# Kernel optimization log

Hardware: AMD Instinct MI355X
Metric: run time of the kernel (lower is better)

Reference implementation:

```python
import jax, jax.numpy as jnp
import numpy as np

N, DIN, DOUT = 8192, 4096, 4096

def setup_inputs() -> dict:
    key = jax.random.key(0)
    k1, k2 = jax.random.split(key)
    x = jax.random.normal(k1, (N, DIN), dtype=jnp.float32)
    # ternary-ish weights; forward applies sign() via STE anyway
    weight = jax.random.normal(k2, (DOUT, DIN), dtype=jnp.float32)
    bias = jnp.zeros((DOUT,), dtype=jnp.float32)
    scale = jnp.ones((1,), dtype=jnp.float32)  # scale_init = 1.0
    return {"x": x, "weight": weight, "bias": bias, "scale": scale}


def reference(x, weight, bias, scale):
    # STE sign-quantization: value is sign(weight) in {-1,0,1},
    # gradient flows to weight as identity.
    w = weight - jax.lax.stop_gradient(weight - jnp.sign(weight))
    # fused ternary matmul + scale + bias: out = scale * (x @ w.T + bias)
    # (backward in the torch code scales grad for x, w, AND bias, implying
    #  bias sits inside the scale multiplier)
    return scale[0] * (jnp.matmul(x, w.T) + bias)
```

## Files before the change

### kernel.cpp

```cpp
#include <hip/hip_runtime.h>
#include <hip/hip_bf16.h>
#include <stdint.h>

#define M_DIM 8192
#define K_DIM 4096
#define N_DIM 4096

typedef int intx4  __attribute__((ext_vector_type(4)));
typedef int intx16 __attribute__((ext_vector_type(16)));

__global__ void cvt_fused_i8_kernel(const float* __restrict__ x,
                                    const float* __restrict__ w,
                                    signed char* __restrict__ xb,
                                    signed char* __restrict__ wb,
                                    float* __restrict__ row_scale) {
    const int b   = blockIdx.x;
    const int tid = threadIdx.x;
    if (b < M_DIM) {
        __shared__ float wmax[4];
        const float* xr = x + (size_t)b * K_DIM;
        float4 v[4];
#pragma unroll
        for (int i = 0; i < 4; ++i)
            v[i] = *(const float4*)(xr + tid * 4 + i * 1024);

        float am = 0.f;
#pragma unroll
        for (int i = 0; i < 4; ++i) {
            am = fmaxf(am, fabsf(v[i].x)); am = fmaxf(am, fabsf(v[i].y));
            am = fmaxf(am, fabsf(v[i].z)); am = fmaxf(am, fabsf(v[i].w));
        }
#pragma unroll
        for (int off = 32; off > 0; off >>= 1)
            am = fmaxf(am, __shfl_xor(am, off));
        if ((tid & 63) == 0) wmax[tid >> 6] = am;
        __syncthreads();
        am = fmaxf(fmaxf(wmax[0], wmax[1]), fmaxf(wmax[2], wmax[3]));
        am = fmaxf(am, 1e-30f);

        const float inv = 127.f / am;
#pragma unroll
        for (int i = 0; i < 4; ++i) {
            union { signed char c[4]; uint32_t u; } r;
            const float* vf = (const float*)&v[i];
#pragma unroll
            for (int k = 0; k < 4; ++k) {
                int q = (int)rintf(vf[k] * inv);
                q = q > 127 ? 127 : (q < -127 ? -127 : q);
                r.c[k] = (signed char)q;
            }
            *(uint32_t*)(xb + (size_t)b * K_DIM + tid * 4 + i * 1024) = r.u;
        }
        if (tid == 0) row_scale[b] = am * (1.f / 127.f);
    } else {
        size_t t = ((size_t)(b - M_DIM) * blockDim.x + tid) * 8;
        float4 a = *(const float4*)(w + t);
        float4 c = *(const float4*)(w + t + 4);
        union { signed char s[8]; uint2 u; } r;
        r.s[0] = (a.x > 0.f) - (a.x < 0.f); r.s[1] = (a.y > 0.f) - (a.y < 0.f);
        r.s[2] = (a.z > 0.f) - (a.z < 0.f); r.s[3] = (a.w > 0.f) - (a.w < 0.f);
        r.s[4] = (c.x > 0.f) - (c.x < 0.f); r.s[5] = (c.y > 0.f) - (c.y < 0.f);
        r.s[6] = (c.z > 0.f) - (c.z < 0.f); r.s[7] = (c.w > 0.f) - (c.w < 0.f);
        *(uint2*)(wb + t) = r.u;
    }
}

__device__ __forceinline__ void gld_lds16(const void* g, void* l) {
    __builtin_amdgcn_global_load_lds(
        (const __attribute__((address_space(1))) void*)g,
        (__attribute__((address_space(3))) void*)l,
        16, 0, 0);
}

__global__ void __launch_bounds__(512, 2)
gemm_i8_kernel(const signed char* __restrict__ A,
               const signed char* __restrict__ B,
               const float* __restrict__ bias,
               const float* __restrict__ scale,
               const float* __restrict__ row_scale,
               float* __restrict__ out) {
    __shared__ __attribute__((aligned(16))) signed char sA[3][256 * 64];
    __shared__ __attribute__((aligned(16))) signed char sB[3][256 * 64];

    const int tid  = threadIdx.x;
    const int lane = tid & 63;
    const int wave = tid >> 6;
    const int wm = wave >> 2;
    const int wn = wave & 3;
    const int r5 = lane & 31;
    const int hi = lane >> 5;

    const int bid = blockIdx.x;
    const int swz = (bid & 7) * 64 + (bid >> 3);
    const int rowBase = (swz >> 4) * 256;
    const int colBase = (swz & 15) * 256;

    const int sc   = (lane & 3) ^ ((lane >> 3) & 3) ^ ((wave & 1) << 1);
    const int srow = wave * 16 + (lane >> 2);
    const signed char* gA0 = A + (size_t)(rowBase + srow) * K_DIM + sc * 16;
    const signed char* gA1 = gA0 + (size_t)128 * K_DIM;
    const signed char* gB0 = B + (size_t)(colBase + srow) * K_DIM + sc * 16;
    const signed char* gB1 = gB0 + (size_t)128 * K_DIM;
    const int ldsR0 = wave * 1024;
    const int ldsR1 = 8192 + wave * 1024;

    const int fsw = ((r5 >> 1) & 3) ^ (((r5 >> 4) & 1) << 1);
    const int ckE = ((hi + 0) ^ fsw) * 16;
    const int ckO = ((hi + 2) ^ fsw) * 16;
    const int aOff = (wm * 128 + r5) * 64;
    const int bOff = (wn * 64 + r5) * 64;

    intx16 acc[4][2] = {};

#pragma unroll
    for (int s = 0; s < 2; ++s) {
        const size_t kg = (size_t)s * 64;
        gld_lds16(gA0 + kg, &sA[s][ldsR0]);
        gld_lds16(gA1 + kg, &sA[s][ldsR1]);
        gld_lds16(gB0 + kg, &sB[s][ldsR0]);
        gld_lds16(gB1 + kg, &sB[s][ldsR1]);
    }
    asm volatile("s_waitcnt vmcnt(4)" ::: "memory");
    __builtin_amdgcn_s_barrier();

    int sr = 0;
    int sw = 2;
    for (int t = 0; t < 64; ++t) {
        const signed char* sAb = sA[sr];
        const signed char* sBb = sB[sr];

        intx4 fa[4], fb[2];
#pragma unroll
        for (int mt = 0; mt < 4; ++mt)
            fa[mt] = *(const intx4*)(sAb + aOff + mt * 2048 + ckE);
#pragma unroll
        for (int nt = 0; nt < 2; ++nt)
            fb[nt] = *(const intx4*)(sBb + bOff + nt * 2048 + ckE);
        __builtin_amdgcn_sched_barrier(0);

        intx4 oa[4], ob[2];
#pragma unroll
        for (int mt = 0; mt < 4; ++mt)
            oa[mt] = *(const intx4*)(sAb + aOff + mt * 2048 + ckO);
#pragma unroll
        for (int nt = 0; nt < 2; ++nt)
            ob[nt] = *(const intx4*)(sBb + bOff + nt * 2048 + ckO);
        if (t <= 61) {
            const size_t kg = (size_t)(t + 2) * 64;
            gld_lds16(gA0 + kg, &sA[sw][ldsR0]);
            gld_lds16(gA1 + kg, &sA[sw][ldsR1]);
            gld_lds16(gB0 + kg, &sB[sw][ldsR0]);
            gld_lds16(gB1 + kg, &sB[sw][ldsR1]);
        }
        __builtin_amdgcn_sched_barrier(0);

        __builtin_amdgcn_s_setprio(1);
#pragma unroll
        for (int mt = 0; mt < 4; ++mt)
#pragma unroll
            for (int nt = 0; nt < 2; ++nt)
                acc[mt][nt] = __builtin_amdgcn_mfma_i32_32x32x32_i8(
                    fa[mt], fb[nt], acc[mt][nt], 0, 0, 0);
        __builtin_amdgcn_s_setprio(0);
        __builtin_amdgcn_sched_barrier(0);

        __builtin_amdgcn_s_setprio(1);
#pragma unroll
        for (int mt = 0; mt < 4; ++mt)
#pragma unroll
            for (int nt = 0; nt < 2; ++nt)
                acc[mt][nt] = __builtin_amdgcn_mfma_i32_32x32x32_i8(
                    oa[mt], ob[nt], acc[mt][nt], 0, 0, 0);
        __builtin_amdgcn_s_setprio(0);
        __builtin_amdgcn_sched_barrier(0);

        if (t <= 61)      asm volatile("s_waitcnt vmcnt(4)" ::: "memory");
        else if (t == 62) asm volatile("s_waitcnt vmcnt(0)" ::: "memory");
        __builtin_amdgcn_s_barrier();

        sr = (sr == 2) ? 0 : sr + 1;
        sw = (sw == 2) ? 0 : sw + 1;
    }

    const float s = scale[0];
#pragma unroll
    for (int nt = 0; nt < 2; ++nt) {
        const int gcol = colBase + wn * 64 + nt * 32 + r5;
        const float bv = bias[gcol];
#pragma unroll
        for (int mt = 0; mt < 4; ++mt) {
#pragma unroll
            for (int q = 0; q < 4; ++q) {
                const int row0 = rowBase + wm * 128 + mt * 32 + q * 8 + hi * 4;
                const float4 rs4 = *(const float4*)(row_scale + row0);
                const float rs[4] = {rs4.x, rs4.y, rs4.z, rs4.w};
#pragma unroll
                for (int r = 0; r < 4; ++r)
                    __builtin_nontemporal_store(
                        s * ((float)acc[mt][nt][q * 4 + r] * rs[r] + bv),
                        out + (size_t)(row0 + r) * N_DIM + gcol);
            }
        }
    }
}

__global__ void fallback_kernel(const float* __restrict__ x,
                                const float* __restrict__ w,
                                const float* __restrict__ bias,
                                const float* __restrict__ scale,
                                float* __restrict__ out) {
    int col = blockIdx.x * 64 + (threadIdx.x & 63);
    int row = blockIdx.y * 4 + (threadIdx.x >> 6);
    const float* xr = x + (size_t)row * K_DIM;
    const float* wr = w + (size_t)col * K_DIM;
    float acc = 0.f;
    for (int k = 0; k < K_DIM; k += 4) {
        float4 a = *(const float4*)(xr + k);
        float4 b = *(const float4*)(wr + k);
        acc += a.x * (b.x > 0.f ? 1.f : (b.x < 0.f ? -1.f : 0.f));
        acc += a.y * (b.y > 0.f ? 1.f : (b.y < 0.f ? -1.f : 0.f));
        acc += a.z * (b.z > 0.f ? 1.f : (b.z < 0.f ? -1.f : 0.f));
        acc += a.w * (b.w > 0.f ? 1.f : (b.w < 0.f ? -1.f : 0.f));
    }
    out[(size_t)row * N_DIM + col] = scale[0] * (acc + bias[col]);
}

extern "C" void kernel_launch(void* const* d_in, const int* in_sizes, int n_in,
                              void* d_out, int out_size, void* d_ws, size_t ws_size,
                              hipStream_t stream) {
    const float* x     = (const float*)d_in[0];
    const float* w     = (const float*)d_in[1];
    const float* bias  = (const float*)d_in[2];
    const float* scale = (const float*)d_in[3];
    float* out = (float*)d_out;

    const size_t xb_bytes = (size_t)M_DIM * K_DIM;
    const size_t wb_bytes = (size_t)N_DIM * K_DIM;
    const size_t need = xb_bytes + wb_bytes + M_DIM * sizeof(float);

    if (ws_size >= need) {
        signed char* xb = (signed char*)d_ws;
        signed char* wb = xb + xb_bytes;
        float* row_scale = (float*)(wb + wb_bytes);
        const unsigned w_blocks = (unsigned)((size_t)N_DIM * K_DIM / 8 / 256);
        cvt_fused_i8_kernel<<<dim3(M_DIM + w_blocks), 256, 0, stream>>>(
            x, w, xb, wb, row_scale);
        gemm_i8_kernel<<<dim3((M_DIM / 256) * (N_DIM / 256)), 512, 0, stream>>>(
            xb, wb, bias, scale, row_scale, out);
    } else {
        dim3 grid(N_DIM / 64, M_DIM / 4);
        fallback_kernel<<<grid, 256, 0, stream>>>(x, w, bias, scale, out);
    }
}
```

Measured before the change: 395.9 us.

## Use 4 waves per block with 128x128 per-wave tiles in int8 GEMM

The block drops from 8 waves to 4, and each wave now computes a 128x128 output sub-tile (4x4 MFMA tiles) instead of 128x64. This raises register-level reuse of the A and B fragments read from LDS and halves the LDS fragment reads per MFMA. Each thread issues twice as many global-to-LDS loads, with the swizzled loading adjusted to match. It doubles the accumulator registers and lowers occupancy to one block per CU, which may hurt latency hiding.

```diff
diff --git a/kernel.cpp b/kernel.cpp
--- a/kernel.cpp
+++ b/kernel.cpp
@@ -72,7 +72,7 @@
         16, 0, 0);
 }
 
-__global__ void __launch_bounds__(512, 2)
+__global__ void __launch_bounds__(256, 1)
 gemm_i8_kernel(const signed char* __restrict__ A,
                const signed char* __restrict__ B,
                const float* __restrict__ bias,
@@ -85,8 +85,8 @@
     const int tid  = threadIdx.x;
     const int lane = tid & 63;
     const int wave = tid >> 6;
-    const int wm = wave >> 2;
-    const int wn = wave & 3;
+    const int wm = wave >> 1;
+    const int wn = wave & 1;
     const int r5 = lane & 31;
     const int hi = lane >> 5;
 
@@ -95,32 +95,39 @@
     const int rowBase = (swz >> 4) * 256;
     const int colBase = (swz & 15) * 256;
 
-    const int sc   = (lane & 3) ^ ((lane >> 3) & 3) ^ ((wave & 1) << 1);
-    const int srow = wave * 16 + (lane >> 2);
-    const signed char* gA0 = A + (size_t)(rowBase + srow) * K_DIM + sc * 16;
-    const signed char* gA1 = gA0 + (size_t)128 * K_DIM;
-    const signed char* gB0 = B + (size_t)(colBase + srow) * K_DIM + sc * 16;
-    const signed char* gB1 = gB0 + (size_t)128 * K_DIM;
-    const int ldsR0 = wave * 1024;
-    const int ldsR1 = 8192 + wave * 1024;
+    const int scE = (lane & 3) ^ ((lane >> 3) & 3);
+    const int scO = scE ^ 2;
+    const int srow = wave * 64 + (lane >> 2);
+    const signed char* gAe = A + (size_t)(rowBase + srow) * K_DIM + scE * 16;
+    const signed char* gAo = A + (size_t)(rowBase + srow) * K_DIM + scO * 16;
+    const signed char* gBe = B + (size_t)(colBase + srow) * K_DIM + scE * 16;
+    const signed char* gBo = B + (size_t)(colBase + srow) * K_DIM + scO * 16;
+    const int ldsW = (wave * 64) * 64;
+
+#define STAGE(slot, kt)                                                        \
+    do {                                                                       \
+        const size_t kg_ = (size_t)(kt) * 64;                                  \
+        gld_lds16(gAe + kg_,                  &sA[slot][ldsW]);                \
+        gld_lds16(gAo + kg_ + 16 * K_DIM,     &sA[slot][ldsW + 1024]);         \
+        gld_lds16(gAe + kg_ + 32 * K_DIM,     &sA[slot][ldsW + 2048]);         \
+        gld_lds16(gAo + kg_ + 48 * K_DIM,     &sA[slot][ldsW + 3072]);         \
+        gld_lds16(gBe + kg_,                  &sB[slot][ldsW]);                \
+        gld_lds16(gBo + kg_ + 16 * K_DIM,     &sB[slot][ldsW + 1024]);         \
+        gld_lds16(gBe + kg_ + 32 * K_DIM,     &sB[slot][ldsW + 2048]);         \
+        gld_lds16(gBo + kg_ + 48 * K_DIM,     &sB[slot][ldsW + 3072]);         \
+    } while (0)
 
     const int fsw = ((r5 >> 1) & 3) ^ (((r5 >> 4) & 1) << 1);
     const int ckE = ((hi + 0) ^ fsw) * 16;
     const int ckO = ((hi + 2) ^ fsw) * 16;
     const int aOff = (wm * 128 + r5) * 64;
-    const int bOff = (wn * 64 + r5) * 64;
-
-    intx16 acc[4][2] = {};
-
-#pragma unroll
-    for (int s = 0; s < 2; ++s) {
-        const size_t kg = (size_t)s * 64;
-        gld_lds16(gA0 + kg, &sA[s][ldsR0]);
-        gld_lds16(gA1 + kg, &sA[s][ldsR1]);
-        gld_lds16(gB0 + kg, &sB[s][ldsR0]);
-        gld_lds16(gB1 + kg, &sB[s][ldsR1]);
-    }
-    asm volatile("s_waitcnt vmcnt(4)" ::: "memory");
+    const int bOff = (wn * 128 + r5) * 64;
+
+    intx16 acc[4][4] = {};
+
+    STAGE(0, 0);
+    STAGE(1, 1);
+    asm volatile("s_waitcnt vmcnt(8)" ::: "memory");
     __builtin_amdgcn_s_barrier();
 
     int sr = 0;
@@ -129,36 +136,30 @@
         const signed char* sAb = sA[sr];
         const signed char* sBb = sB[sr];
 
-        intx4 fa[4], fb[2];
+        intx4 fa[4], fb[4];
 #pragma unroll
         for (int mt = 0; mt < 4; ++mt)
             fa[mt] = *(const intx4*)(sAb + aOff + mt * 2048 + ckE);
 #pragma unroll
-        for (int nt = 0; nt < 2; ++nt)
+        for (int nt = 0; nt < 4; ++nt)
             fb[nt] = *(const intx4*)(sBb + bOff + nt * 2048 + ckE);
         __builtin_amdgcn_sched_barrier(0);
 
-        intx4 oa[4], ob[2];
+        intx4 oa[4], ob[4];
 #pragma unroll
         for (int mt = 0; mt < 4; ++mt)
             oa[mt] = *(const intx4*)(sAb + aOff + mt * 2048 + ckO);
 #pragma unroll
-        for (int nt = 0; nt < 2; ++nt)
+        for (int nt = 0; nt < 4; ++nt)
             ob[nt] = *(const intx4*)(sBb + bOff + nt * 2048 + ckO);
-        if (t <= 61) {
-            const size_t kg = (size_t)(t + 2) * 64;
-            gld_lds16(gA0 + kg, &sA[sw][ldsR0]);
-            gld_lds16(gA1 + kg, &sA[sw][ldsR1]);
-            gld_lds16(gB0 + kg, &sB[sw][ldsR0]);
-            gld_lds16(gB1 + kg, &sB[sw][ldsR1]);
-        }
+        if (t <= 61) STAGE(sw, t + 2);
         __builtin_amdgcn_sched_barrier(0);
 
         __builtin_amdgcn_s_setprio(1);
 #pragma unroll
         for (int mt = 0; mt < 4; ++mt)
 #pragma unroll
-            for (int nt = 0; nt < 2; ++nt)
+            for (int nt = 0; nt < 4; ++nt)
                 acc[mt][nt] = __builtin_amdgcn_mfma_i32_32x32x32_i8(
                     fa[mt], fb[nt], acc[mt][nt], 0, 0, 0);
         __builtin_amdgcn_s_setprio(0);
@@ -168,36 +169,40 @@
 #pragma unroll
         for (int mt = 0; mt < 4; ++mt)
 #pragma unroll
-            for (int nt = 0; nt < 2; ++nt)
+            for (int nt = 0; nt < 4; ++nt)
                 acc[mt][nt] = __builtin_amdgcn_mfma_i32_32x32x32_i8(
                     oa[mt], ob[nt], acc[mt][nt], 0, 0, 0);
         __builtin_amdgcn_s_setprio(0);
         __builtin_amdgcn_sched_barrier(0);
 
-        if (t <= 61)      asm volatile("s_waitcnt vmcnt(4)" ::: "memory");
+        if (t <= 61)      asm volatile("s_waitcnt vmcnt(8)" ::: "memory");
         else if (t == 62) asm volatile("s_waitcnt vmcnt(0)" ::: "memory");
         __builtin_amdgcn_s_barrier();
 
         sr = (sr == 2) ? 0 : sr + 1;
         sw = (sw == 2) ? 0 : sw + 1;
     }
+#undef STAGE
 
     const float s = scale[0];
-#pragma unroll
-    for (int nt = 0; nt < 2; ++nt) {
-        const int gcol = colBase + wn * 64 + nt * 32 + r5;
-        const float bv = bias[gcol];
-#pragma unroll
-        for (int mt = 0; mt < 4; ++mt) {
-#pragma unroll
-            for (int q = 0; q < 4; ++q) {
-                const int row0 = rowBase + wm * 128 + mt * 32 + q * 8 + hi * 4;
-                const float4 rs4 = *(const float4*)(row_scale + row0);
-                const float rs[4] = {rs4.x, rs4.y, rs4.z, rs4.w};
+    float bv[4];
+#pragma unroll
+    for (int nt = 0; nt < 4; ++nt)
+        bv[nt] = bias[colBase + wn * 128 + nt * 32 + r5];
+#pragma unroll
+    for (int mt = 0; mt < 4; ++mt) {
+#pragma unroll
+        for (int q = 0; q < 4; ++q) {
+            const int row0 = rowBase + wm * 128 + mt * 32 + q * 8 + hi * 4;
+            const float4 rs4 = *(const float4*)(row_scale + row0);
+            const float rs[4] = {rs4.x, rs4.y, rs4.z, rs4.w};
+#pragma unroll
+            for (int nt = 0; nt < 4; ++nt) {
+                const int gcol = colBase + wn * 128 + nt * 32 + r5;
 #pragma unroll
                 for (int r = 0; r < 4; ++r)
                     __builtin_nontemporal_store(
-                        s * ((float)acc[mt][nt][q * 4 + r] * rs[r] + bv),
+                        s * ((float)acc[mt][nt][q * 4 + r] * rs[r] + bv[nt]),
                         out + (size_t)(row0 + r) * N_DIM + gcol);
             }
         }
@@ -245,7 +250,7 @@
         const unsigned w_blocks = (unsigned)((size_t)N_DIM * K_DIM / 8 / 256);
         cvt_fused_i8_kernel<<<dim3(M_DIM + w_blocks), 256, 0, stream>>>(
             x, w, xb, wb, row_scale);
-        gemm_i8_kernel<<<dim3((M_DIM / 256) * (N_DIM / 256)), 512, 0, stream>>>(
+        gemm_i8_kernel<<<dim3((M_DIM / 256) * (N_DIM / 256)), 256, 0, stream>>>(
             xb, wb, bias, scale, row_scale, out);
     } else {
         dim3 grid(N_DIM / 64, M_DIM / 4);
```

After: 447.5 us. +13.0%, slower.
